# Optimization experiments

Measured on AMD Instinct MI355X. Metric: run time of the kernel, lower is better.

Reference implementation:

```python
import jax, jax.numpy as jnp
import numpy as np

# Le-ADMM constants (ADMM_Net init values; V_div_mat / R_div_mat are
# precomputed buffers in the torch code using these, not the learned mus)
MU1_0, MU2_0, MU3_0 = 1e-6, 1e-5, 4e-5
TAU_0 = 1e-4
ITERS = 5
BATCH = 8
SENSOR = (540, 960)


def _pad_full(v, sh):
    # zero-pad sensor-size (..., H, W) to full (..., 2H, 2W), centered
    H, W = sh
    pads = [(0, 0)] * (v.ndim - 2) + [(H // 2, H - H // 2), (W // 2, W - W // 2)]
    return jnp.pad(v, pads)


def _crop(v, sh):
    H, W = sh
    return v[..., H // 2:H // 2 + H, W // 2:W // 2 + W]


def _fft2(v):
    return jnp.fft.fft2(jnp.fft.ifftshift(v, axes=(-2, -1)), axes=(-2, -1))


def _ifft2(V):
    return jnp.fft.fftshift(jnp.fft.ifft2(V, axes=(-2, -1)), axes=(-2, -1))


def _Hop(x, Hf):
    return jnp.real(_ifft2(Hf * _fft2(x)))


def _Hadj(x, Hf):
    return jnp.real(_ifft2(jnp.conj(Hf) * _fft2(x)))


def _Psi(x):
    # forward finite differences (circular), vertical and horizontal
    return jnp.roll(x, 1, axis=-2) - x, jnp.roll(x, 1, axis=-1) - x


def _PsiT(uv, uh):
    return (jnp.roll(uv, -1, axis=-2) - uv) + (jnp.roll(uh, -1, axis=-1) - uh)


def _soft_iso(uv, uh, thresh):
    # isotropic soft-threshold on the 2D gradient magnitude
    mag = jnp.sqrt(uv * uv + uh * uh)
    mult = jnp.maximum(mag - thresh, 0.0) / jnp.maximum(mag, 1e-12)
    return uv * mult, uh * mult


def setup_inputs() -> dict:
    key = jax.random.key(0)
    k1, k2 = jax.random.split(key)
    x = jax.random.uniform(k1, (BATCH,) + SENSOR, dtype=jnp.float32)
    h = jax.random.uniform(k2, SENSOR, dtype=jnp.float32)
    h = h / jnp.linalg.norm(h)  # normalized PSF
    ones = jnp.ones((ITERS,), jnp.float32)
    return {
        "x": x,
        "h": h,
        "mu1": ones * MU1_0,
        "mu2": ones * MU2_0,
        "mu3": ones * MU3_0,
        "tau": ones * TAU_0,
    }


def reference(x, h, mu1, mu2, mu3, tau):
    sh = h.shape  # sensor size (H, W)
    fullH, fullW = 2 * sh[0], 2 * sh[1]

    Hf = _fft2(_pad_full(h[None], sh))[0]  # (2H, 2W) complex
    CtC = _pad_full(jnp.ones((1,) + sh, x.dtype), sh)[0]
    V_div = 1.0 / (CtC + MU1_0)
    lap = jnp.zeros((fullH, fullW), x.dtype)
    lap = (lap.at[0, 0].set(4.0).at[0, 1].set(-1.0).at[1, 0].set(-1.0)
           .at[0, -1].set(-1.0).at[-1, 0].set(-1.0))
    PsiTPsi = jnp.abs(jnp.fft.fft2(lap))
    R_div = 1.0 / (MU1_0 * jnp.abs(Hf) ** 2 + MU2_0 * PsiTPsi + MU3_0)

    Cty = _pad_full(x, sh)  # (B, 2H, 2W)
    zfull = jnp.zeros((x.shape[0], fullH, fullW), x.dtype)

    out = zfull
    for i in range(ITERS):
        # forward() calls admm.restValues() every iteration, so all ADMM state
        # (X, U, V, W, alphas) is zero at the start of each iteration: each
        # iteration is one ADMM step from zero state; output keeps the last.
        X, a1, a2v, a2h, a3 = zfull, zfull, zfull, zfull, zfull
        pv, ph = _Psi(X)
        Uv, Uh = _soft_iso(pv + a2v / mu2[i], ph + a2h / mu2[i], tau[i] / mu2[i])
        V = V_div * (a1 + mu1[i] * _Hop(X, Hf) + Cty)
        W = jnp.maximum(a3 / mu3[i] + X, 0.0)
        r = ((mu3[i] * W - a3)
             + _PsiT(mu2[i] * Uv - a2v, mu2[i] * Uh - a2h)
             + _Hadj(mu1[i] * V - a1, Hf))
        out = jnp.real(_ifft2(R_div * _fft2(r)))
    return _crop(out, sh)
```

## Files before the change

kernel.cpp:

```cpp
#include <hip/hip_runtime.h>


#define PI2 6.2831853071795864f

typedef float v2f __attribute__((ext_vector_type(2)));

__device__ __forceinline__ v2f vmk(float x, float y){ v2f r; r.x = x; r.y = y; return r; }
__device__ __forceinline__ v2f cmul(v2f a, v2f b){
    return vmk(a.x, a.x)*b + vmk(-a.y, a.y)*vmk(b.y, b.x);
}
__device__ __forceinline__ float4 pk(v2f a, v2f b){ return make_float4(a.x,a.y,b.x,b.y); }

__device__ __forceinline__ int IDX(int a){ return a + (a >> 4); }
#define IDXSZ(n) ((n) + ((n) >> 4))
__device__ __forceinline__ int IDXP(int a){ return a + ((a >> 5) << 1); }
#define IDXPSZ(n) ((n) + (((n) >> 5) << 1) + 4)
__device__ __forceinline__ int IDX4(int a){ return a + (a >> 4); }
#define IDX4SZ(n) ((n) + ((n) >> 4) + 2)

__device__ __forceinline__ void ldp(const v2f* __restrict__ b, int pos,
                                    v2f& v0, v2f& v1){
    const float4 t = *(const float4*)&b[IDXP(2*pos)];
    v0 = vmk(t.x,t.y); v1 = vmk(t.z,t.w);
}
__device__ __forceinline__ void stp(v2f* __restrict__ b, int pos,
                                    v2f v0, v2f v1){
    *(float4*)&b[IDXP(2*pos)] = pk(v0, v1);
}
__device__ __forceinline__ void ld4(const float4* __restrict__ b, int pos,
                                    v2f& v0, v2f& v1){
    const float4 t = b[IDX4(pos)];
    v0 = vmk(t.x,t.y); v1 = vmk(t.z,t.w);
}
__device__ __forceinline__ void st4(float4* __restrict__ b, int pos,
                                    v2f v0, v2f v1){
    b[IDX4(pos)] = pk(v0, v1);
}
__device__ __forceinline__ void ld4g(const float4* __restrict__ b, int pos, int g,
                                     v2f& v0, v2f& v1){
    const float4 t = b[IDX4(2*pos+g)];
    v0 = vmk(t.x,t.y); v1 = vmk(t.z,t.w);
}
__device__ __forceinline__ void st4g(float4* __restrict__ b, int pos, int g,
                                     v2f v0, v2f v1){
    b[IDX4(2*pos+g)] = pk(v0, v1);
}

template<int DIR>
__device__ __forceinline__ void dft3(v2f x0, v2f x1, v2f x2,
                                     v2f& y0, v2f& y1, v2f& y2)
{
    constexpr float s3 = (float)DIR * 0.8660254037844386f;
    v2f t = x1 + x2, u = x1 - x2;
    v2f m = x0 - 0.5f*t;
    v2f iu = vmk(-s3*u.y, s3*u.x);
    y0 = x0 + t; y1 = m + iu; y2 = m - iu;
}

template<int DIR>
__device__ __forceinline__ void dft4(v2f a0, v2f a1, v2f a2, v2f a3,
                                     v2f& b0, v2f& b1, v2f& b2, v2f& b3)
{
    v2f t0 = a0+a2, t1 = a0-a2, t2 = a1+a3, t3 = a1-a3;
    v2f j3 = vmk(-(float)DIR*t3.y, (float)DIR*t3.x);
    b0 = t0+t2; b2 = t0-t2; b1 = t1+j3; b3 = t1-j3;
}

template<int DIR>
__device__ __forceinline__ void dft6(const v2f a[6], v2f b[6])
{
    v2f e0,e1,e2,o0,o1,o2;
    dft3<DIR>(a[0],a[2],a[4], e0,e1,e2);
    dft3<DIR>(a[1],a[3],a[5], o0,o1,o2);
    constexpr float s3 = (float)DIR * 0.8660254037844386f;
    const v2f w1 = vmk( 0.5f, s3);
    const v2f w2 = vmk(-0.5f, s3);
    v2f t1 = cmul(w1,o1), t2 = cmul(w2,o2);
    b[0]=e0+o0; b[3]=e0-o0;
    b[1]=e1+t1; b[4]=e1-t1;
    b[2]=e2+t2; b[5]=e2-t2;
}

template<int DIR>
__device__ __forceinline__ void dft8(const v2f a[8], v2f b[8])
{
    v2f e0,e1,e2,e3,o0,o1,o2,o3;
    dft4<DIR>(a[0],a[2],a[4],a[6], e0,e1,e2,e3);
    dft4<DIR>(a[1],a[3],a[5],a[7], o0,o1,o2,o3);
    constexpr float c = 0.70710678118654752f;
    const v2f w1 = vmk( c, (float)DIR*c);
    const v2f w3 = vmk(-c, (float)DIR*c);
    v2f t1 = cmul(w1,o1);
    v2f t2 = vmk(-(float)DIR*o2.y, (float)DIR*o2.x);
    v2f t3 = cmul(w3,o3);
    b[0]=e0+o0; b[4]=e0-o0;
    b[1]=e1+t1; b[5]=e1-t1;
    b[2]=e2+t2; b[6]=e2-t2;
    b[3]=e3+t3; b[7]=e3-t3;
}

template<int DIR>
__device__ __forceinline__ void dft5(const v2f a[5], v2f b[5])
{
    constexpr float C1 = 0.30901699437494742f, S1c = 0.9510565162951535f;
    constexpr float C2 = -0.8090169943749475f, S2c = 0.5877852522924731f;
    v2f t1 = a[1]+a[4], t2 = a[2]+a[3], d1 = a[1]-a[4], d2 = a[2]-a[3];
    v2f m1 = a[0] + C1*t1 + C2*t2;
    v2f m2 = a[0] + C2*t1 + C1*t2;
    v2f e1 = S1c*d1 + S2c*d2;
    v2f e2 = S2c*d1 - S1c*d2;
    v2f ie1 = vmk(-(float)DIR*e1.y, (float)DIR*e1.x);
    v2f ie2 = vmk(-(float)DIR*e2.y, (float)DIR*e2.x);
    b[0] = a[0] + t1 + t2;
    b[1] = m1+ie1; b[4] = m1-ie1;
    b[2] = m2+ie2; b[3] = m2-ie2;
}

template<int DIR>
__device__ __forceinline__ void dft9(const v2f a[9], v2f b[9])
{
    v2f C0[3], C1[3], C2[3];
    dft3<DIR>(a[0],a[3],a[6], C0[0],C0[1],C0[2]);
    dft3<DIR>(a[1],a[4],a[7], C1[0],C1[1],C1[2]);
    dft3<DIR>(a[2],a[5],a[8], C2[0],C2[1],C2[2]);
    const v2f w91 = vmk(0.7660444431189780f, (float)DIR*0.6427876096865393f);
    const v2f w92 = vmk(0.1736481776669304f, (float)DIR*0.9848077530122081f);
    const v2f w94 = vmk(-0.9396926207859084f, (float)DIR*0.3420201433256687f);
    C1[1]=cmul(C1[1],w91); C1[2]=cmul(C1[2],w92);
    C2[1]=cmul(C2[1],w92); C2[2]=cmul(C2[2],w94);
    dft3<DIR>(C0[0],C1[0],C2[0], b[0],b[3],b[6]);
    dft3<DIR>(C0[1],C1[1],C2[1], b[1],b[4],b[7]);
    dft3<DIR>(C0[2],C1[2],C2[2], b[2],b[5],b[8]);
}

template<int DIR>
__device__ __forceinline__ void dft10(const v2f a[10], v2f b[10])
{
    v2f ae[5] = {a[0],a[2],a[4],a[6],a[8]};
    v2f ao[5] = {a[1],a[3],a[5],a[7],a[9]};
    v2f E[5], O[5];
    dft5<DIR>(ae, E); dft5<DIR>(ao, O);
    const v2f w1 = vmk( 0.8090169943749475f, (float)DIR*0.5877852522924731f);
    const v2f w2 = vmk( 0.3090169943749474f, (float)DIR*0.9510565162951535f);
    const v2f w3 = vmk(-0.3090169943749474f, (float)DIR*0.9510565162951535f);
    const v2f w4 = vmk(-0.8090169943749475f, (float)DIR*0.5877852522924731f);
    v2f t1 = cmul(O[1],w1), t2 = cmul(O[2],w2), t3 = cmul(O[3],w3), t4 = cmul(O[4],w4);
    b[0]=E[0]+O[0]; b[5]=E[0]-O[0];
    b[1]=E[1]+t1;   b[6]=E[1]-t1;
    b[2]=E[2]+t2;   b[7]=E[2]-t2;
    b[3]=E[3]+t3;   b[8]=E[3]-t3;
    b[4]=E[4]+t4;   b[9]=E[4]-t4;
}

template<int DIR>
__device__ __forceinline__ void dft12(const v2f a[12], v2f b[12])
{
    v2f C0[4], C1[4], C2[4];
    dft4<DIR>(a[0],a[3],a[6],a[9],  C0[0],C0[1],C0[2],C0[3]);
    dft4<DIR>(a[1],a[4],a[7],a[10], C1[0],C1[1],C1[2],C1[3]);
    dft4<DIR>(a[2],a[5],a[8],a[11], C2[0],C2[1],C2[2],C2[3]);
    const v2f w121 = vmk(0.8660254037844386f, (float)DIR*0.5f);
    const v2f w122 = vmk(0.5f, (float)DIR*0.8660254037844386f);
    const v2f w124 = vmk(-0.5f, (float)DIR*0.8660254037844386f);
    C1[1]=cmul(C1[1],w121); C1[2]=cmul(C1[2],w122);
    C1[3]=vmk(-(float)DIR*C1[3].y, (float)DIR*C1[3].x);
    C2[1]=cmul(C2[1],w122); C2[2]=cmul(C2[2],w124);
    C2[3]=-C2[3];
    dft3<DIR>(C0[0],C1[0],C2[0], b[0],b[4],b[8]);
    dft3<DIR>(C0[1],C1[1],C2[1], b[1],b[5],b[9]);
    dft3<DIR>(C0[2],C1[2],C2[2], b[2],b[6],b[10]);
    dft3<DIR>(C0[3],C1[3],C2[3], b[3],b[7],b[11]);
}


__device__ __forceinline__ void row_s1_fwd_h(const float* __restrict__ xa,
                                             v2f* __restrict__ bA, int tid)
{
    constexpr float STEP = -PI2 / 1920.0f;
    const v2f z = vmk(0.f,0.f);
    for (int p = tid; p < 240; p += 256) {
        v2f a[8], b[8];
        a[0]=z; a[1]=z; a[6]=z; a[7]=z;
        a[2] = vmk(xa[p],     0.f);
        a[3] = vmk(xa[p+240], 0.f);
        a[4] = vmk(xa[p+480], 0.f);
        a[5] = vmk(xa[p+720], 0.f);
        dft8<-1>(a,b);
        float sv, cv; __sincosf(STEP * (float)p, &sv, &cv);
        v2f w1 = vmk(cv, sv), w = w1;
        b[1] = cmul(b[1], w);
        #pragma unroll
        for (int u = 2; u < 8; ++u) { w = cmul(w, w1); b[u] = cmul(b[u], w); }
        #pragma unroll
        for (int u = 0; u < 8; ++u) bA[IDX(8*p + u)] = b[u];
    }
}

template<int DIR, int R, int NCUR, int S>
__device__ __forceinline__ void mid_stage(const v2f* __restrict__ src,
                                          v2f* __restrict__ dst, int tid)
{
    constexpr int M  = NCUR / R;
    constexpr int NB = M * S;
    constexpr float STEP = (float)DIR * PI2 / (float)NCUR;
    for (int i = tid; i < NB; i += 256) {
        const int p = i / S;
        v2f a[R], b[R];
        #pragma unroll
        for (int t = 0; t < R; ++t) a[t] = src[IDX(i + S*M*t)];
        if constexpr (R == 6) dft6<DIR>(a,b); else dft8<DIR>(a,b);
        float sv, cv; __sincosf(STEP * (float)p, &sv, &cv);
        v2f w1 = vmk(cv, sv), w = w1;
        b[1] = cmul(b[1], w);
        #pragma unroll
        for (int u = 2; u < R; ++u) { w = cmul(w, w1); b[u] = cmul(b[u], w); }
        const int ob = (i - p*S) + S*(R*p);
        #pragma unroll
        for (int u = 0; u < R; ++u) dst[IDX(ob + S*u)] = b[u];
    }
}

__device__ __forceinline__ void row_fin5_store_h(const v2f* __restrict__ src,
                                                 v2f* __restrict__ gdst, int tid)
{
    for (int q = tid; q < 384; q += 256) {
        v2f a[5], b[5];
        #pragma unroll
        for (int u = 0; u < 5; ++u) a[u] = src[IDX(q + 384*u)];
        dft5<-1>(a,b);
        #pragma unroll
        for (int u = 0; u < 5; ++u) gdst[q + 384*u] = b[u];
    }
}


__device__ __forceinline__ void rp_s1_fwd(const float* __restrict__ xa,
                                          const float* __restrict__ xb,
                                          float4* __restrict__ sb, int tid)
{
    constexpr float STEP = -PI2 / 1920.0f;
    const v2f z = vmk(0.f,0.f);
    for (int p = tid; p < 240; p += 256) {
        v2f a0[8], a1[8], b0[8], b1[8];
        a0[0]=a0[1]=a0[6]=a0[7]=z; a1[0]=a1[1]=a1[6]=a1[7]=z;
        #pragma unroll
        for (int t = 0; t < 4; ++t) {
            a0[2+t] = vmk(xa[p+240*t],     xb[p+240*t]);
            a1[2+t] = vmk(xa[960+p+240*t], xb[960+p+240*t]);
        }
        dft8<-1>(a0,b0); dft8<-1>(a1,b1);
        float sv, cv; __sincosf(STEP*(float)p, &sv, &cv);
        v2f w1 = vmk(cv,sv), w = w1;
        b0[1]=cmul(b0[1],w); b1[1]=cmul(b1[1],w);
        #pragma unroll
        for (int u = 2; u < 8; ++u){ w = cmul(w,w1); b0[u]=cmul(b0[u],w); b1[u]=cmul(b1[u],w); }
        #pragma unroll
        for (int u = 0; u < 8; ++u) st4(sb, 8*p+u, b0[u], b1[u]);
    }
}

__device__ __forceinline__ void rp_s1_inv(const v2f* __restrict__ Zr0,
                                          const v2f* __restrict__ Zr1,
                                          float4* __restrict__ sb, int tid)
{
    constexpr float STEP = PI2 / 1920.0f;
    for (int p = tid; p < 240; p += 256) {
        v2f a0[8], a1[8], b0[8], b1[8];
        #pragma unroll
        for (int t = 0; t < 8; ++t) { a0[t] = Zr0[p+240*t]; a1[t] = Zr1[p+240*t]; }
        dft8<1>(a0,b0); dft8<1>(a1,b1);
        float sv, cv; __sincosf(STEP*(float)p, &sv, &cv);
        v2f w1 = vmk(cv,sv), w = w1;
        b0[1]=cmul(b0[1],w); b1[1]=cmul(b1[1],w);
        #pragma unroll
        for (int u = 2; u < 8; ++u){ w = cmul(w,w1); b0[u]=cmul(b0[u],w); b1[u]=cmul(b1[u],w); }
        #pragma unroll
        for (int u = 0; u < 8; ++u) st4(sb, 8*p+u, b0[u], b1[u]);
    }
}

template<int DIR>
__device__ __forceinline__ void rp_mid8_ip(float4* __restrict__ sb, int tid)
{
    constexpr float STEP = (float)DIR * PI2 / 240.0f;
    const bool act = tid < 240;
    v2f b0[8], b1[8]; int ob = 0;
    if (act) {
        const int p = tid >> 3;
        v2f a0[8], a1[8];
        #pragma unroll
        for (int t = 0; t < 8; ++t) ld4(sb, tid + 240*t, a0[t], a1[t]);
        dft8<DIR>(a0,b0); dft8<DIR>(a1,b1);
        float sv, cv; __sincosf(STEP*(float)p, &sv, &cv);
        v2f w1 = vmk(cv,sv), w = w1;
        b0[1]=cmul(b0[1],w); b1[1]=cmul(b1[1],w);
        #pragma unroll
        for (int u = 2; u < 8; ++u){ w = cmul(w,w1); b0[u]=cmul(b0[u],w); b1[u]=cmul(b1[u],w); }
        ob = (tid - 8*p) + 64*p;
    }
    __syncthreads();
    if (act) {
        #pragma unroll
        for (int u = 0; u < 8; ++u) st4(sb, ob + 8*u, b0[u], b1[u]);
    }
    __syncthreads();
}

template<int DIR>
__device__ __forceinline__ void rp_mid6_ip(float4* __restrict__ sb, int tid)
{
    constexpr float STEP = (float)DIR * PI2 / 30.0f;
    v2f c0[6], c1[6], d0[6], d1[6]; int ob0, ob1 = 0;
    {
        const int i = tid, p = i >> 6;
        v2f a0[6], a1[6];
        #pragma unroll
        for (int t = 0; t < 6; ++t) ld4(sb, i + 320*t, a0[t], a1[t]);
        dft6<DIR>(a0,c0); dft6<DIR>(a1,c1);
        float sv, cv; __sincosf(STEP*(float)p, &sv, &cv);
        v2f w1 = vmk(cv,sv), w = w1;
        c0[1]=cmul(c0[1],w); c1[1]=cmul(c1[1],w);
        #pragma unroll
        for (int u = 2; u < 6; ++u){ w = cmul(w,w1); c0[u]=cmul(c0[u],w); c1[u]=cmul(c1[u],w); }
        ob0 = (i - 64*p) + 384*p;
    }
    const bool act2 = tid < 64;
    if (act2) {
        const int i = 256 + tid;
        v2f a0[6], a1[6];
        #pragma unroll
        for (int t = 0; t < 6; ++t) ld4(sb, i + 320*t, a0[t], a1[t]);
        dft6<DIR>(a0,d0); dft6<DIR>(a1,d1);
        float sv, cv; __sincosf(STEP*4.0f, &sv, &cv);
        v2f w1 = vmk(cv,sv), w = w1;
        d0[1]=cmul(d0[1],w); d1[1]=cmul(d1[1],w);
        #pragma unroll
        for (int u = 2; u < 6; ++u){ w = cmul(w,w1); d0[u]=cmul(d0[u],w); d1[u]=cmul(d1[u],w); }
        ob1 = tid + 1536;
    }
    __syncthreads();
    {
        #pragma unroll
        for (int u = 0; u < 6; ++u) st4(sb, ob0 + 64*u, c0[u], c1[u]);
    }
    if (act2) {
        #pragma unroll
        for (int u = 0; u < 6; ++u) st4(sb, ob1 + 64*u, d0[u], d1[u]);
    }
    __syncthreads();
}

__device__ __forceinline__ void rp_fin5_storeZ(const float4* __restrict__ sb,
                                               v2f* __restrict__ Zr0,
                                               v2f* __restrict__ Zr1, int tid)
{
    for (int q = tid; q < 384; q += 256) {
        v2f a0[5],a1[5],b0[5],b1[5];
        #pragma unroll
        for (int u = 0; u < 5; ++u) ld4(sb, q + 384*u, a0[u], a1[u]);
        dft5<-1>(a0,b0); dft5<-1>(a1,b1);
        #pragma unroll
        for (int u = 0; u < 5; ++u) { Zr0[q+384*u] = b0[u]; Zr1[q+384*u] = b1[u]; }
    }
}

__device__ __forceinline__ void rp_fin5_crop(const float4* __restrict__ sb,
                                             float* __restrict__ oa0, float* __restrict__ ob0,
                                             float* __restrict__ oa1, float* __restrict__ ob1,
                                             int tid)
{
    for (int q = tid; q < 384; q += 256) {
        v2f a0[5],a1[5],b0[5],b1[5];
        #pragma unroll
        for (int u = 0; u < 5; ++u) ld4(sb, q + 384*u, a0[u], a1[u]);
        dft5<1>(a0,b0); dft5<1>(a1,b1);
        oa0[q+480] = b0[0].x; ob0[q+480] = b0[0].y;
        oa1[q+480] = b1[0].x; ob1[q+480] = b1[0].y;
        if (q < 96)   { oa0[q+864] = b0[1].x; ob0[q+864] = b0[1].y;
                        oa1[q+864] = b1[1].x; ob1[q+864] = b1[1].y; }
        if (q >= 288) { oa0[q-288] = b0[3].x; ob0[q-288] = b0[3].y;
                        oa1[q-288] = b1[3].x; ob1[q-288] = b1[3].y; }
        oa0[q+96]  = b0[4].x; ob0[q+96]  = b0[4].y;
        oa1[q+96]  = b1[4].x; ob1[q+96]  = b1[4].y;
    }
}


__device__ __forceinline__ void col_s1_fwd_pair(const v2f* __restrict__ g, int c0,
                                                v2f* __restrict__ bA, int tid)
{
    constexpr float STEP = -PI2 / 1080.0f;
    const v2f z = vmk(0.f,0.f);
    const float4* gc = (const float4*)(g + c0);
    for (int p = tid; p < 180; p += 256) {
        v2f a0[6], a1[6], b0[6], b1[6];
        a0[0]=a0[5]=a1[0]=a1[5]=z;
        if (p >= 90) { float4 t = gc[(p-90)*960]; a0[1]=vmk(t.x,t.y); a1[1]=vmk(t.z,t.w); }
        else         { a0[1]=a1[1]=z; }
        { float4 t = gc[(p+90)*960];  a0[2]=vmk(t.x,t.y); a1[2]=vmk(t.z,t.w); }
        { float4 t = gc[(p+270)*960]; a0[3]=vmk(t.x,t.y); a1[3]=vmk(t.z,t.w); }
        if (p < 90)  { float4 t = gc[(p+450)*960]; a0[4]=vmk(t.x,t.y); a1[4]=vmk(t.z,t.w); }
        else         { a0[4]=a1[4]=z; }
        dft6<-1>(a0,b0); dft6<-1>(a1,b1);
        float sv, cv; __sincosf(STEP*(float)p, &sv, &cv);
        v2f w1 = vmk(cv,sv), w = w1;
        b0[1]=cmul(b0[1],w); b1[1]=cmul(b1[1],w);
        #pragma unroll
        for (int u = 2; u < 6; ++u){ w = cmul(w,w1); b0[u]=cmul(b0[u],w); b1[u]=cmul(b1[u],w); }
        #pragma unroll
        for (int u = 0; u < 6; ++u) stp(bA, 6*p + u, b0[u], b1[u]);
    }
}

template<int DIR, int NCUR, int SC>
__device__ __forceinline__ void mid_pair(const v2f* __restrict__ src,
                                         v2f* __restrict__ dst, int tid)
{
    constexpr int NB = 180;
    constexpr float STEP = (float)DIR * PI2 / (float)NCUR;
    for (int ic = tid; ic < NB; ic += 256) {
        const int p = ic / SC;
        v2f a0[6], a1[6], b0[6], b1[6];
        #pragma unroll
        for (int t = 0; t < 6; ++t) ldp(src, ic + NB*t, a0[t], a1[t]);
        dft6<DIR>(a0,b0); dft6<DIR>(a1,b1);
        float sv, cv; __sincosf(STEP*(float)p, &sv, &cv);
        v2f w1 = vmk(cv,sv), w = w1;
        b0[1]=cmul(b0[1],w); b1[1]=cmul(b1[1],w);
        #pragma unroll
        for (int u = 2; u < 6; ++u){ w = cmul(w,w1); b0[u]=cmul(b0[u],w); b1[u]=cmul(b1[u],w); }
        const int ob = (ic - p*SC) + SC*6*p;
        #pragma unroll
        for (int u = 0; u < 6; ++u) stp(dst, ob + SC*u, b0[u], b1[u]);
    }
}


__device__ __forceinline__ void c4_s1_fwd10(const v2f* __restrict__ Zp, int c0,
                                            float4* __restrict__ sb, int tid)
{
    constexpr float STEP = -PI2 / 1080.0f;
    const v2f z = vmk(0.f,0.f);
    const float4* gc = (const float4*)(Zp + c0);
    const bool act = tid < 216;
    if (act) {
        const int g = tid & 1, p = tid >> 1;
        v2f a0[10], a1[10], b0[10], b1[10];
        a0[0]=a0[1]=a0[8]=a0[9]=z; a1[0]=a1[1]=a1[8]=a1[9]=z;
        if (p >= 54) { float4 t = gc[(p-54)*960+g]; a0[2]=vmk(t.x,t.y); a1[2]=vmk(t.z,t.w); }
        else         { a0[2]=a1[2]=z; }
        { float4 t = gc[(p+54)*960+g];  a0[3]=vmk(t.x,t.y); a1[3]=vmk(t.z,t.w); }
        { float4 t = gc[(p+162)*960+g]; a0[4]=vmk(t.x,t.y); a1[4]=vmk(t.z,t.w); }
        { float4 t = gc[(p+270)*960+g]; a0[5]=vmk(t.x,t.y); a1[5]=vmk(t.z,t.w); }
        { float4 t = gc[(p+378)*960+g]; a0[6]=vmk(t.x,t.y); a1[6]=vmk(t.z,t.w); }
        if (p < 54)  { float4 t = gc[(p+486)*960+g]; a0[7]=vmk(t.x,t.y); a1[7]=vmk(t.z,t.w); }
        else         { a0[7]=a1[7]=z; }
        dft10<-1>(a0,b0); dft10<-1>(a1,b1);
        float sv, cv; __sincosf(STEP*(float)p, &sv, &cv);
        v2f w1 = vmk(cv,sv), w = w1;
        b0[1]=cmul(b0[1],w); b1[1]=cmul(b1[1],w);
        #pragma unroll
        for (int u = 2; u < 10; ++u){ w = cmul(w,w1); b0[u]=cmul(b0[u],w); b1[u]=cmul(b1[u],w); }
        #pragma unroll
        for (int u = 0; u < 10; ++u) st4g(sb, 10*p+u, g, b0[u], b1[u]);
    }
    __syncthreads();
}

template<int DIR, int NCUR, int SC>
__device__ __forceinline__ void c4_mid12_ip(float4* __restrict__ sb, int tid)
{
    constexpr int NB = (NCUR/12)*SC;
    constexpr float STEP = (float)DIR * PI2 / (float)NCUR;
    const bool act = tid < 2*NB;
    v2f b0[12], b1[12]; int ob = 0, g = 0;
    if (act) {
        g = tid & 1;
        const int ic = tid >> 1;
        const int p = ic / SC;
        v2f a0[12], a1[12];
        #pragma unroll
        for (int t = 0; t < 12; ++t) ld4g(sb, ic + NB*t, g, a0[t], a1[t]);
        dft12<DIR>(a0,b0); dft12<DIR>(a1,b1);
        float sv, cv; __sincosf(STEP*(float)p, &sv, &cv);
        v2f w1 = vmk(cv,sv), w = w1;
        b0[1]=cmul(b0[1],w); b1[1]=cmul(b1[1],w);
        #pragma unroll
        for (int u = 2; u < 12; ++u){ w = cmul(w,w1); b0[u]=cmul(b0[u],w); b1[u]=cmul(b1[u],w); }
        ob = (ic - p*SC) + SC*12*p;
    }
    __syncthreads();
    if (act) {
        #pragma unroll
        for (int u = 0; u < 12; ++u) st4g(sb, ob + SC*u, g, b0[u], b1[u]);
    }
    __syncthreads();
}

__device__ __forceinline__ void c4_f9K9_ip(float4* __restrict__ sb,
                                           const float4* __restrict__ KI,
                                           int cg, int tid)
{
    constexpr float STEP = PI2 / 1080.0f;
    const bool act = tid < 240;
    v2f d0[9], d1[9]; int q = 0, g = 0;
    if (act) {
        g = tid & 1; q = tid >> 1;
        const float4* Kc = KI + (cg*2 + g)*1080;
        v2f a0[9], a1[9], s0[9], s1[9];
        #pragma unroll
        for (int u = 0; u < 9; ++u) ld4g(sb, q + 120*u, g, a0[u], a1[u]);
        dft9<-1>(a0,s0); dft9<-1>(a1,s1);
        #pragma unroll
        for (int u = 0; u < 9; ++u) {
            float4 kk = Kc[q + 120*u];
            s0[u] = cmul(s0[u], vmk(kk.x,kk.y));
            s1[u] = cmul(s1[u], vmk(kk.z,kk.w));
        }
        dft9<1>(s0,d0); dft9<1>(s1,d1);
        float sv, cv; __sincosf(STEP*(float)q, &sv, &cv);
        v2f w1 = vmk(cv,sv), w = w1;
        d0[1]=cmul(d0[1],w); d1[1]=cmul(d1[1],w);
        #pragma unroll
        for (int u = 2; u < 9; ++u){ w = cmul(w,w1); d0[u]=cmul(d0[u],w); d1[u]=cmul(d1[u],w); }
    }
    __syncthreads();
    if (act) {
        #pragma unroll
        for (int u = 0; u < 9; ++u) st4g(sb, 9*q + u, g, d0[u], d1[u]);
    }
    __syncthreads();
}

__device__ __forceinline__ void c4_fin10_crop(const float4* __restrict__ sb,
                                              v2f* __restrict__ Zp,
                                              int c0, int tid)
{
    const bool act = tid < 216;
    if (!act) return;
    const int g = tid & 1, q = tid >> 1;
    float4* gc = (float4*)(Zp + c0);
    v2f a0[10], a1[10], b0[10], b1[10];
    #pragma unroll
    for (int u = 0; u < 10; ++u) ld4g(sb, q + 108*u, g, a0[u], a1[u]);
    dft10<1>(a0,b0); dft10<1>(a1,b1);
    gc[(q+270)*960+g] = pk(b0[0], b1[0]);
    gc[(q+378)*960+g] = pk(b0[1], b1[1]);
    if (q < 54)  gc[(q+486)*960+g] = pk(b0[2], b1[2]);
    if (q >= 54) gc[(q-54)*960+g]  = pk(b0[7], b1[7]);
    gc[(q+54)*960+g]  = pk(b0[8], b1[8]);
    gc[(q+162)*960+g] = pk(b0[9], b1[9]);
}


__global__ __launch_bounds__(256,5) void k_row_fwd(const float* __restrict__ x,
                                                   const float* __restrict__ h,
                                                   v2f* __restrict__ Z,
                                                   v2f* __restrict__ Hrow)
{
    __shared__ float4 sb[IDX4SZ(1920)];
    const int tid = threadIdx.x;
    if (blockIdx.x < 1080) {
        const int pp = blockIdx.x / 270;
        const int r0 = (blockIdx.x % 270) * 2;
        const float* xa = x + ((2*pp  )*540 + r0)*960;
        const float* xb = x + ((2*pp+1)*540 + r0)*960;
        rp_s1_fwd(xa, xb, sb, tid); __syncthreads();
        rp_mid8_ip<-1>(sb, tid);
        rp_mid6_ip<-1>(sb, tid);
        v2f* Zr0 = Z + (pp*540 + r0)*1920;
        rp_fin5_storeZ(sb, Zr0, Zr0 + 1920, tid);
    } else {
        v2f* bA = (v2f*)sb;
        v2f* bB = bA + IDXSZ(1920);
        const int r = blockIdx.x - 1080;
        row_s1_fwd_h(h + r*960, bA, tid); __syncthreads();
        mid_stage<-1,8,240, 8>(bA, bB, tid); __syncthreads();
        mid_stage<-1,6, 30,64>(bB, bA, tid); __syncthreads();
        row_fin5_store_h(bA, Hrow + r*1920, tid);
    }
}

__global__ __launch_bounds__(256,4) void k_col_fft_h_buildK(const v2f* __restrict__ Hrow,
                                                            const float* __restrict__ mu1,
                                                            float4* __restrict__ KI)
{
    __shared__ v2f bA[IDXPSZ(2160)], bB[IDXPSZ(2160)];
    const int tid = threadIdx.x;
    const int xcd = blockIdx.x & 7, idx = blockIdx.x >> 3;
    const int cpair = xcd*120 + idx, c0 = cpair*2;
    col_s1_fwd_pair(Hrow, c0, bA, tid);  __syncthreads();
    mid_pair<-1,180, 6>(bA, bB, tid);    __syncthreads();
    mid_pair<-1, 30,36>(bB, bA, tid);    __syncthreads();
    const float sc = mu1[4] / ((1.0f + 1e-6f) * 2073600.0f);
    const float cos0 = __cosf(PI2 * (float)(c0  ) * (1.0f/1920.0f));
    const float cos1 = __cosf(PI2 * (float)(c0+1) * (1.0f/1920.0f));
    float4* Kc = KI + cpair*1080;
    for (int p = tid; p < 216; p += 256) {
        v2f a0[5],a1[5],b0[5],b1[5];
        #pragma unroll
        for (int u = 0; u < 5; ++u) ldp(bA, p + 216*u, a0[u], a1[u]);
        dft5<-1>(a0,b0); dft5<-1>(a1,b1);
        #pragma unroll
        for (int u = 0; u < 5; ++u) {
            const int k = p + 216*u;
            const float cosk = __cosf(PI2 * (float)k * (1.0f/1080.0f));
            float m0 = b0[u].x*b0[u].x + b0[u].y*b0[u].y;
            float m1 = b1[u].x*b1[u].x + b1[u].y*b1[u].y;
            float f0 = sc / (1e-6f*m0 + 1e-5f*(4.0f - 2.0f*cosk - 2.0f*cos0) + 4e-5f);
            float f1 = sc / (1e-6f*m1 + 1e-5f*(4.0f - 2.0f*cosk - 2.0f*cos1) + 4e-5f);
            Kc[k] = make_float4(f0*b0[u].x, -f0*b0[u].y, f1*b1[u].x, -f1*b1[u].y);
        }
    }
}

__global__ __launch_bounds__(256,4) void k_col_fused(v2f* __restrict__ Z,
                                                     const float4* __restrict__ KI)
{
    __shared__ float4 sb[IDX4SZ(2160)];
    const int tid = threadIdx.x;
    const int xcd = blockIdx.x & 7, idx = blockIdx.x >> 3;
    const int pp  = idx / 60;
    const int cg  = xcd*60 + (idx - pp*60);
    const int c0  = cg*4;
    v2f* Zp = Z + pp*540*1920;
    c4_s1_fwd10(Zp, c0, sb, tid);
    c4_mid12_ip<-1,108,10>(sb, tid);
    c4_f9K9_ip(sb, KI, cg, tid);
    c4_mid12_ip< 1,120, 9>(sb, tid);
    c4_fin10_crop(sb, Zp, c0, tid);
}

__global__ __launch_bounds__(256,5) void k_row_inv_out(const v2f* __restrict__ Z,
                                                       float* __restrict__ out)
{
    __shared__ float4 sb[IDX4SZ(1920)];
    const int tid = threadIdx.x;
    const int pp = blockIdx.x / 270;
    const int r0 = (blockIdx.x % 270) * 2;
    const v2f* Zr0 = Z + (pp*540 + r0)*1920;
    rp_s1_inv(Zr0, Zr0 + 1920, sb, tid); __syncthreads();
    rp_mid8_ip<1>(sb, tid);
    rp_mid6_ip<1>(sb, tid);
    float* oa0 = out + ((2*pp  )*540 + r0)*960;
    float* ob0 = out + ((2*pp+1)*540 + r0)*960;
    rp_fin5_crop(sb, oa0, ob0, oa0 + 960, ob0 + 960, tid);
}

extern "C" void kernel_launch(void* const* d_in, const int* in_sizes, int n_in,
                              void* d_out, int out_size, void* d_ws, size_t ws_size,
                              hipStream_t stream)
{
    (void)in_sizes; (void)n_in; (void)out_size; (void)ws_size;
    const float* x   = (const float*)d_in[0];
    const float* h   = (const float*)d_in[1];
    const float* mu1 = (const float*)d_in[2];
    float*       out = (float*)d_out;

    float4* KI   = (float4*)d_ws;
    v2f*    Z    = (v2f*)(KI + 960*1080);
    v2f*    Hrow = Z + 4*540*1920;

    k_row_fwd         <<<1620,   256, 0, stream>>>(x, h, Z, Hrow);
    k_col_fft_h_buildK<<<960,    256, 0, stream>>>(Hrow, mu1, KI);
    k_col_fused       <<<1920,   256, 0, stream>>>(Z, KI);
    k_row_inv_out     <<<1080,   256, 0, stream>>>(Z, out);
}
```

Measured before the change: 73.63 us.

## Restructure row FFTs as 12x16x10 with four rows per block

Row forward and inverse FFT kernels now process four rows per block (two packed complex pairs) and factor the 1920-point transform as radix 12, 16, 10 instead of 8, 8, 6, 5. This removes one LDS pass and its barriers and halves the number of blocks. In exchange, shared memory per block doubles, launch bounds drop to 2 blocks per SM, and the larger radix needs more registers, so occupancy falls.

```diff
diff --git a/kernel.cpp b/kernel.cpp
--- a/kernel.cpp
+++ b/kernel.cpp
@@ -26,15 +26,6 @@
 __device__ __forceinline__ void stp(v2f* __restrict__ b, int pos,
                                     v2f v0, v2f v1){
     *(float4*)&b[IDXP(2*pos)] = pk(v0, v1);
-}
-__device__ __forceinline__ void ld4(const float4* __restrict__ b, int pos,
-                                    v2f& v0, v2f& v1){
-    const float4 t = b[IDX4(pos)];
-    v0 = vmk(t.x,t.y); v1 = vmk(t.z,t.w);
-}
-__device__ __forceinline__ void st4(float4* __restrict__ b, int pos,
-                                    v2f v0, v2f v1){
-    b[IDX4(pos)] = pk(v0, v1);
 }
 __device__ __forceinline__ void ld4g(const float4* __restrict__ b, int pos, int g,
                                      v2f& v0, v2f& v1){
@@ -172,6 +163,30 @@
     dft3<DIR>(C0[3],C1[3],C2[3], b[3],b[7],b[11]);
 }
 
+template<int DIR>
+__device__ __forceinline__ void dft16(const v2f a[16], v2f b[16])
+{
+    v2f C0[4], C1[4], C2[4], C3[4];
+    dft4<DIR>(a[0],a[4],a[8], a[12], C0[0],C0[1],C0[2],C0[3]);
+    dft4<DIR>(a[1],a[5],a[9], a[13], C1[0],C1[1],C1[2],C1[3]);
+    dft4<DIR>(a[2],a[6],a[10],a[14], C2[0],C2[1],C2[2],C2[3]);
+    dft4<DIR>(a[3],a[7],a[11],a[15], C3[0],C3[1],C3[2],C3[3]);
+    const v2f w1 = vmk(0.9238795325112867f, (float)DIR*0.3826834323650898f);
+    const v2f w2 = vmk(0.7071067811865476f, (float)DIR*0.7071067811865476f);
+    const v2f w3 = vmk(0.3826834323650898f, (float)DIR*0.9238795325112867f);
+    const v2f w6 = vmk(-0.7071067811865476f, (float)DIR*0.7071067811865476f);
+    const v2f w9 = vmk(-0.9238795325112867f, -(float)DIR*0.3826834323650898f);
+    C1[1]=cmul(C1[1],w1); C1[2]=cmul(C1[2],w2); C1[3]=cmul(C1[3],w3);
+    C2[1]=cmul(C2[1],w2);
+    C2[2]=vmk(-(float)DIR*C2[2].y, (float)DIR*C2[2].x);
+    C2[3]=cmul(C2[3],w6);
+    C3[1]=cmul(C3[1],w3); C3[2]=cmul(C3[2],w6); C3[3]=cmul(C3[3],w9);
+    dft4<DIR>(C0[0],C1[0],C2[0],C3[0], b[0],b[4],b[8], b[12]);
+    dft4<DIR>(C0[1],C1[1],C2[1],C3[1], b[1],b[5],b[9], b[13]);
+    dft4<DIR>(C0[2],C1[2],C2[2],C3[2], b[2],b[6],b[10],b[14]);
+    dft4<DIR>(C0[3],C1[3],C2[3],C3[3], b[3],b[7],b[11],b[15]);
+}
+
 
 __device__ __forceinline__ void row_s1_fwd_h(const float* __restrict__ xa,
                                              v2f* __restrict__ bA, int tid)
@@ -234,154 +249,130 @@
 }
 
 
-__device__ __forceinline__ void rp_s1_fwd(const float* __restrict__ xa,
+__device__ __forceinline__ void rq_s1_fwd(const float* __restrict__ xa,
                                           const float* __restrict__ xb,
                                           float4* __restrict__ sb, int tid)
 {
     constexpr float STEP = -PI2 / 1920.0f;
     const v2f z = vmk(0.f,0.f);
-    for (int p = tid; p < 240; p += 256) {
-        v2f a0[8], a1[8], b0[8], b1[8];
-        a0[0]=a0[1]=a0[6]=a0[7]=z; a1[0]=a1[1]=a1[6]=a1[7]=z;
-        #pragma unroll
-        for (int t = 0; t < 4; ++t) {
-            a0[2+t] = vmk(xa[p+240*t],     xb[p+240*t]);
-            a1[2+t] = vmk(xa[960+p+240*t], xb[960+p+240*t]);
+    for (int it = tid; it < 320; it += 256) {
+        const int g = (it < 160) ? 0 : 1;
+        const int p = it - 160*g;
+        const float* xa0 = xa + (2*g)*960;
+        const float* xb0 = xb + (2*g)*960;
+        v2f a0[12], a1[12], b0[12], b1[12];
+        a0[0]=a0[1]=a0[2]=a0[9]=a0[10]=a0[11]=z;
+        a1[0]=a1[1]=a1[2]=a1[9]=a1[10]=a1[11]=z;
+        #pragma unroll
+        for (int s = 0; s < 6; ++s) {
+            a0[3+s] = vmk(xa0[p+160*s],     xb0[p+160*s]);
+            a1[3+s] = vmk(xa0[960+p+160*s], xb0[960+p+160*s]);
         }
-        dft8<-1>(a0,b0); dft8<-1>(a1,b1);
+        dft12<-1>(a0,b0); dft12<-1>(a1,b1);
         float sv, cv; __sincosf(STEP*(float)p, &sv, &cv);
         v2f w1 = vmk(cv,sv), w = w1;
         b0[1]=cmul(b0[1],w); b1[1]=cmul(b1[1],w);
         #pragma unroll
-        for (int u = 2; u < 8; ++u){ w = cmul(w,w1); b0[u]=cmul(b0[u],w); b1[u]=cmul(b1[u],w); }
-        #pragma unroll
-        for (int u = 0; u < 8; ++u) st4(sb, 8*p+u, b0[u], b1[u]);
-    }
-}
-
-__device__ __forceinline__ void rp_s1_inv(const v2f* __restrict__ Zr0,
-                                          const v2f* __restrict__ Zr1,
+        for (int u = 2; u < 12; ++u){ w = cmul(w,w1); b0[u]=cmul(b0[u],w); b1[u]=cmul(b1[u],w); }
+        #pragma unroll
+        for (int u = 0; u < 12; ++u) st4g(sb, 12*p+u, g, b0[u], b1[u]);
+    }
+}
+
+__device__ __forceinline__ void rq_s1_inv(const v2f* __restrict__ Zbase,
                                           float4* __restrict__ sb, int tid)
 {
     constexpr float STEP = PI2 / 1920.0f;
-    for (int p = tid; p < 240; p += 256) {
-        v2f a0[8], a1[8], b0[8], b1[8];
-        #pragma unroll
-        for (int t = 0; t < 8; ++t) { a0[t] = Zr0[p+240*t]; a1[t] = Zr1[p+240*t]; }
-        dft8<1>(a0,b0); dft8<1>(a1,b1);
+    for (int it = tid; it < 320; it += 256) {
+        const int g = (it < 160) ? 0 : 1;
+        const int p = it - 160*g;
+        const v2f* Zr0 = Zbase + (2*g)*1920;
+        const v2f* Zr1 = Zr0 + 1920;
+        v2f a0[12], a1[12], b0[12], b1[12];
+        #pragma unroll
+        for (int t = 0; t < 12; ++t) { a0[t] = Zr0[p+160*t]; a1[t] = Zr1[p+160*t]; }
+        dft12<1>(a0,b0); dft12<1>(a1,b1);
         float sv, cv; __sincosf(STEP*(float)p, &sv, &cv);
         v2f w1 = vmk(cv,sv), w = w1;
         b0[1]=cmul(b0[1],w); b1[1]=cmul(b1[1],w);
         #pragma unroll
-        for (int u = 2; u < 8; ++u){ w = cmul(w,w1); b0[u]=cmul(b0[u],w); b1[u]=cmul(b1[u],w); }
-        #pragma unroll
-        for (int u = 0; u < 8; ++u) st4(sb, 8*p+u, b0[u], b1[u]);
-    }
-}
-
-template<int DIR>
-__device__ __forceinline__ void rp_mid8_ip(float4* __restrict__ sb, int tid)
-{
-    constexpr float STEP = (float)DIR * PI2 / 240.0f;
+        for (int u = 2; u < 12; ++u){ w = cmul(w,w1); b0[u]=cmul(b0[u],w); b1[u]=cmul(b1[u],w); }
+        #pragma unroll
+        for (int u = 0; u < 12; ++u) st4g(sb, 12*p+u, g, b0[u], b1[u]);
+    }
+}
+
+template<int DIR>
+__device__ __forceinline__ void rq_mid16_ip(float4* __restrict__ sb, int tid)
+{
+    constexpr float STEP = (float)DIR * PI2 / 160.0f;
     const bool act = tid < 240;
-    v2f b0[8], b1[8]; int ob = 0;
+    v2f b0[16], b1[16]; int ob = 0, g = 0;
     if (act) {
-        const int p = tid >> 3;
-        v2f a0[8], a1[8];
-        #pragma unroll
-        for (int t = 0; t < 8; ++t) ld4(sb, tid + 240*t, a0[t], a1[t]);
-        dft8<DIR>(a0,b0); dft8<DIR>(a1,b1);
+        g = (tid < 120) ? 0 : 1;
+        const int ic = tid - 120*g;
+        const int p = ic / 12;
+        v2f a0[16], a1[16];
+        #pragma unroll
+        for (int t = 0; t < 16; ++t) ld4g(sb, ic + 120*t, g, a0[t], a1[t]);
+        dft16<DIR>(a0,b0); dft16<DIR>(a1,b1);
         float sv, cv; __sincosf(STEP*(float)p, &sv, &cv);
         v2f w1 = vmk(cv,sv), w = w1;
         b0[1]=cmul(b0[1],w); b1[1]=cmul(b1[1],w);
         #pragma unroll
-        for (int u = 2; u < 8; ++u){ w = cmul(w,w1); b0[u]=cmul(b0[u],w); b1[u]=cmul(b1[u],w); }
-        ob = (tid - 8*p) + 64*p;
+        for (int u = 2; u < 16; ++u){ w = cmul(w,w1); b0[u]=cmul(b0[u],w); b1[u]=cmul(b1[u],w); }
+        ob = (ic - 12*p) + 192*p;
     }
     __syncthreads();
     if (act) {
         #pragma unroll
-        for (int u = 0; u < 8; ++u) st4(sb, ob + 8*u, b0[u], b1[u]);
+        for (int u = 0; u < 16; ++u) st4g(sb, ob + 12*u, g, b0[u], b1[u]);
     }
     __syncthreads();
 }
 
-template<int DIR>
-__device__ __forceinline__ void rp_mid6_ip(float4* __restrict__ sb, int tid)
-{
-    constexpr float STEP = (float)DIR * PI2 / 30.0f;
-    v2f c0[6], c1[6], d0[6], d1[6]; int ob0, ob1 = 0;
-    {
-        const int i = tid, p = i >> 6;
-        v2f a0[6], a1[6];
-        #pragma unroll
-        for (int t = 0; t < 6; ++t) ld4(sb, i + 320*t, a0[t], a1[t]);
-        dft6<DIR>(a0,c0); dft6<DIR>(a1,c1);
-        float sv, cv; __sincosf(STEP*(float)p, &sv, &cv);
-        v2f w1 = vmk(cv,sv), w = w1;
-        c0[1]=cmul(c0[1],w); c1[1]=cmul(c1[1],w);
-        #pragma unroll
-        for (int u = 2; u < 6; ++u){ w = cmul(w,w1); c0[u]=cmul(c0[u],w); c1[u]=cmul(c1[u],w); }
-        ob0 = (i - 64*p) + 384*p;
-    }
-    const bool act2 = tid < 64;
-    if (act2) {
-        const int i = 256 + tid;
-        v2f a0[6], a1[6];
-        #pragma unroll
-        for (int t = 0; t < 6; ++t) ld4(sb, i + 320*t, a0[t], a1[t]);
-        dft6<DIR>(a0,d0); dft6<DIR>(a1,d1);
-        float sv, cv; __sincosf(STEP*4.0f, &sv, &cv);
-        v2f w1 = vmk(cv,sv), w = w1;
-        d0[1]=cmul(d0[1],w); d1[1]=cmul(d1[1],w);
-        #pragma unroll
-        for (int u = 2; u < 6; ++u){ w = cmul(w,w1); d0[u]=cmul(d0[u],w); d1[u]=cmul(d1[u],w); }
-        ob1 = tid + 1536;
-    }
-    __syncthreads();
-    {
-        #pragma unroll
-        for (int u = 0; u < 6; ++u) st4(sb, ob0 + 64*u, c0[u], c1[u]);
-    }
-    if (act2) {
-        #pragma unroll
-        for (int u = 0; u < 6; ++u) st4(sb, ob1 + 64*u, d0[u], d1[u]);
-    }
-    __syncthreads();
-}
-
-__device__ __forceinline__ void rp_fin5_storeZ(const float4* __restrict__ sb,
-                                               v2f* __restrict__ Zr0,
-                                               v2f* __restrict__ Zr1, int tid)
-{
-    for (int q = tid; q < 384; q += 256) {
-        v2f a0[5],a1[5],b0[5],b1[5];
-        #pragma unroll
-        for (int u = 0; u < 5; ++u) ld4(sb, q + 384*u, a0[u], a1[u]);
-        dft5<-1>(a0,b0); dft5<-1>(a1,b1);
-        #pragma unroll
-        for (int u = 0; u < 5; ++u) { Zr0[q+384*u] = b0[u]; Zr1[q+384*u] = b1[u]; }
-    }
-}
-
-__device__ __forceinline__ void rp_fin5_crop(const float4* __restrict__ sb,
-                                             float* __restrict__ oa0, float* __restrict__ ob0,
-                                             float* __restrict__ oa1, float* __restrict__ ob1,
-                                             int tid)
-{
-    for (int q = tid; q < 384; q += 256) {
-        v2f a0[5],a1[5],b0[5],b1[5];
-        #pragma unroll
-        for (int u = 0; u < 5; ++u) ld4(sb, q + 384*u, a0[u], a1[u]);
-        dft5<1>(a0,b0); dft5<1>(a1,b1);
+__device__ __forceinline__ void rq_fin10_storeZ(const float4* __restrict__ sb,
+                                                v2f* __restrict__ Zbase, int tid)
+{
+    for (int it = tid; it < 384; it += 256) {
+        const int g = (it < 192) ? 0 : 1;
+        const int q = it - 192*g;
+        v2f* Zr0 = Zbase + (2*g)*1920;
+        v2f* Zr1 = Zr0 + 1920;
+        v2f a0[10],a1[10],b0[10],b1[10];
+        #pragma unroll
+        for (int u = 0; u < 10; ++u) ld4g(sb, q + 192*u, g, a0[u], a1[u]);
+        dft10<-1>(a0,b0); dft10<-1>(a1,b1);
+        #pragma unroll
+        for (int u = 0; u < 10; ++u) { Zr0[q+192*u] = b0[u]; Zr1[q+192*u] = b1[u]; }
+    }
+}
+
+__device__ __forceinline__ void rq_fin10_crop(const float4* __restrict__ sb,
+                                              float* __restrict__ oa, float* __restrict__ ob,
+                                              int tid)
+{
+    for (int it = tid; it < 384; it += 256) {
+        const int g = (it < 192) ? 0 : 1;
+        const int q = it - 192*g;
+        float* oa0 = oa + (2*g)*960; float* ob0 = ob + (2*g)*960;
+        float* oa1 = oa0 + 960;      float* ob1 = ob0 + 960;
+        v2f a0[10],a1[10],b0[10],b1[10];
+        #pragma unroll
+        for (int u = 0; u < 10; ++u) ld4g(sb, q + 192*u, g, a0[u], a1[u]);
+        dft10<1>(a0,b0); dft10<1>(a1,b1);
         oa0[q+480] = b0[0].x; ob0[q+480] = b0[0].y;
         oa1[q+480] = b1[0].x; ob1[q+480] = b1[0].y;
-        if (q < 96)   { oa0[q+864] = b0[1].x; ob0[q+864] = b0[1].y;
-                        oa1[q+864] = b1[1].x; ob1[q+864] = b1[1].y; }
-        if (q >= 288) { oa0[q-288] = b0[3].x; ob0[q-288] = b0[3].y;
-                        oa1[q-288] = b1[3].x; ob1[q-288] = b1[3].y; }
-        oa0[q+96]  = b0[4].x; ob0[q+96]  = b0[4].y;
-        oa1[q+96]  = b1[4].x; ob1[q+96]  = b1[4].y;
+        oa0[q+672] = b0[1].x; ob0[q+672] = b0[1].y;
+        oa1[q+672] = b1[1].x; ob1[q+672] = b1[1].y;
+        if (q < 96)  { oa0[q+864] = b0[2].x; ob0[q+864] = b0[2].y;
+                       oa1[q+864] = b1[2].x; ob1[q+864] = b1[2].y; }
+        if (q >= 96) { oa0[q-96]  = b0[7].x; ob0[q-96]  = b0[7].y;
+                       oa1[q-96]  = b1[7].x; ob1[q-96]  = b1[7].y; }
+        oa0[q+96]  = b0[8].x; ob0[q+96]  = b0[8].y;
+        oa1[q+96]  = b1[8].x; ob1[q+96]  = b1[8].y;
+        oa0[q+288] = b0[9].x; ob0[q+288] = b0[9].y;
+        oa1[q+288] = b1[9].x; ob1[q+288] = b1[9].y;
     }
 }
 
@@ -553,27 +544,25 @@
 }
 
 
-__global__ __launch_bounds__(256,5) void k_row_fwd(const float* __restrict__ x,
+__global__ __launch_bounds__(256,2) void k_row_fwd(const float* __restrict__ x,
                                                    const float* __restrict__ h,
                                                    v2f* __restrict__ Z,
                                                    v2f* __restrict__ Hrow)
 {
-    __shared__ float4 sb[IDX4SZ(1920)];
+    __shared__ float4 sb[IDX4SZ(3840)];
     const int tid = threadIdx.x;
-    if (blockIdx.x < 1080) {
-        const int pp = blockIdx.x / 270;
-        const int r0 = (blockIdx.x % 270) * 2;
+    if (blockIdx.x < 540) {
+        const int pp = blockIdx.x / 135;
+        const int r0 = (blockIdx.x % 135) * 4;
         const float* xa = x + ((2*pp  )*540 + r0)*960;
         const float* xb = x + ((2*pp+1)*540 + r0)*960;
-        rp_s1_fwd(xa, xb, sb, tid); __syncthreads();
-        rp_mid8_ip<-1>(sb, tid);
-        rp_mid6_ip<-1>(sb, tid);
-        v2f* Zr0 = Z + (pp*540 + r0)*1920;
-        rp_fin5_storeZ(sb, Zr0, Zr0 + 1920, tid);
+        rq_s1_fwd(xa, xb, sb, tid); __syncthreads();
+        rq_mid16_ip<-1>(sb, tid);
+        rq_fin10_storeZ(sb, Z + (pp*540 + r0)*1920, tid);
     } else {
         v2f* bA = (v2f*)sb;
         v2f* bB = bA + IDXSZ(1920);
-        const int r = blockIdx.x - 1080;
+        const int r = blockIdx.x - 540;
         row_s1_fwd_h(h + r*960, bA, tid); __syncthreads();
         mid_stage<-1,8,240, 8>(bA, bB, tid); __syncthreads();
         mid_stage<-1,6, 30,64>(bB, bA, tid); __syncthreads();
@@ -631,20 +620,16 @@
     c4_fin10_crop(sb, Zp, c0, tid);
 }
 
-__global__ __launch_bounds__(256,5) void k_row_inv_out(const v2f* __restrict__ Z,
+__global__ __launch_bounds__(256,2) void k_row_inv_out(const v2f* __restrict__ Z,
                                                        float* __restrict__ out)
 {
-    __shared__ float4 sb[IDX4SZ(1920)];
+    __shared__ float4 sb[IDX4SZ(3840)];
     const int tid = threadIdx.x;
-    const int pp = blockIdx.x / 270;
-    const int r0 = (blockIdx.x % 270) * 2;
-    const v2f* Zr0 = Z + (pp*540 + r0)*1920;
-    rp_s1_inv(Zr0, Zr0 + 1920, sb, tid); __syncthreads();
-    rp_mid8_ip<1>(sb, tid);
-    rp_mid6_ip<1>(sb, tid);
-    float* oa0 = out + ((2*pp  )*540 + r0)*960;
-    float* ob0 = out + ((2*pp+1)*540 + r0)*960;
-    rp_fin5_crop(sb, oa0, ob0, oa0 + 960, ob0 + 960, tid);
+    const int pp = blockIdx.x / 135;
+    const int r0 = (blockIdx.x % 135) * 4;
+    rq_s1_inv(Z + (pp*540 + r0)*1920, sb, tid); __syncthreads();
+    rq_mid16_ip<1>(sb, tid);
+    rq_fin10_crop(sb, out + ((2*pp)*540 + r0)*960, out + ((2*pp+1)*540 + r0)*960, tid);
 }
 
 extern "C" void kernel_launch(void* const* d_in, const int* in_sizes, int n_in,
@@ -661,8 +646,8 @@
     v2f*    Z    = (v2f*)(KI + 960*1080);
     v2f*    Hrow = Z + 4*540*1920;
 
-    k_row_fwd         <<<1620,   256, 0, stream>>>(x, h, Z, Hrow);
+    k_row_fwd         <<<1080,   256, 0, stream>>>(x, h, Z, Hrow);
     k_col_fft_h_buildK<<<960,    256, 0, stream>>>(Hrow, mu1, KI);
     k_col_fused       <<<1920,   256, 0, stream>>>(Z, KI);
-    k_row_inv_out     <<<1080,   256, 0, stream>>>(Z, out);
-}
+    k_row_inv_out     <<<540,    256, 0, stream>>>(Z, out);
+}
```

Result: slower. 80.65 us (+9.5%).
